# Performance work log

Hardware: AMD Instinct MI355X
Metric: run time of the kernel (lower is better)

## Reference

```python
import jax, jax.numpy as jnp
import numpy as np
from jax import lax

R = 1
EPS = 1e-4
K = 2 * R + 1


def _dir_kernels(r):
    k = 2 * r + 1
    ones = np.ones((k, k), np.float32)
    L = ones.copy(); L[:, r + 1:] = 0
    Rk = ones.copy(); Rk[:, :r] = 0
    U = ones.copy(); U[r + 1:, :] = 0
    D = ones.copy(); D[:r, :] = 0
    # NW/NE/SW/SE clone U/D BEFORE normalization (as in the torch code)
    NW = U.copy(); NW[:, r + 1:] = 0
    NE = U.copy(); NE[:, :r] = 0
    SW = D.copy(); SW[:, r + 1:] = 0
    SE = D.copy(); SE[:, :r] = 0
    half = (r + 1) * k          # normalizer for half windows
    quad = (r + 1) ** 2         # normalizer for quadrant windows
    L, Rk, U, D = L / half, Rk / half, U / half, D / half
    NW, NE, SW, SE = NW / quad, NE / quad, SW / quad, SE / quad
    return jnp.asarray(np.stack([L, Rk, U, D, NW, NE, SW, SE])[:, None])  # [8,1,k,k]


_DN = ('NCHW', 'OIHW', 'NCHW')


def _boxfilter(x, r):
    # replication pad + depthwise ones/(k*k) box filter; x: [N,3,H,W]
    k = 2 * r + 1
    xp = jnp.pad(x, ((0, 0), (0, 0), (r, r), (r, r)), mode='edge')
    w = jnp.full((3, 1, k, k), 1.0 / (k * k), dtype=x.dtype)
    return lax.conv_general_dilated(xp, w, (1, 1), 'VALID',
                                    dimension_numbers=_DN, feature_group_count=3)


def setup_inputs() -> dict:
    key = jax.random.key(0)
    k1, k2, k3 = jax.random.split(key, 3)
    lr_x = jax.random.uniform(k1, (1, 3, 2048, 2048), jnp.float32) * 255.0
    lr_y = jax.random.uniform(k2, (1, 3, 2048, 2048), jnp.float32) * 255.0
    hr_x = jax.random.uniform(k3, (1, 3, 4096, 4096), jnp.float32) * 255.0
    return {"lr_x": lr_x, "lr_y": lr_y, "hr_x": hr_x}


def reference(lr_x, lr_y, hr_x):
    # guided-filter coefficients on the low-res pair
    mean_x = _boxfilter(lr_x, R)
    mean_y = _boxfilter(lr_y, R)
    cov_xy = _boxfilter(lr_x * lr_y, R) - mean_x * mean_y
    var_x = _boxfilter(lr_x * lr_x, R) - mean_x * mean_x
    A = cov_xy / (var_x + EPS)            # [1,3,H,W]
    b = mean_y - A * mean_x               # [1,3,H,W]

    # treat channels as batch: [3,1,H,W]; 8 directional kernels at once
    Wd = _dir_kernels(R)                  # [8,1,k,k]
    A_ = A[0][:, None]
    b_ = b[0][:, None]
    im = lr_x[0][:, None]                 # [3,1,H,W]
    pad = [(R, R), (R, R)]
    convA = lax.conv_general_dilated(A_, Wd, (1, 1), pad, dimension_numbers=_DN)
    convb = lax.conv_general_dilated(b_, Wd, (1, 1), pad, dimension_numbers=_DN)
    d = convA * im + convb - im           # [3,8,H,W] directional residuals

    idx = jnp.argmin(jnp.abs(d), axis=1, keepdims=True)   # [3,1,H,W]
    dm = jnp.take_along_axis(d, idx, axis=1)              # best residual
    res = (dm + im).transpose(1, 0, 2, 3)                 # [1,3,H,W]
    # .int() truncation then clamp to [0,255], back to float
    return jnp.clip(jnp.trunc(res), 0.0, 255.0)
```

## Files before the change

### kernel.cpp

```cpp
#include <hip/hip_runtime.h>
#include <math.h>


#define TX 64
#define TY 16
#define SW (TX + 4)
#define SH (TY + 4)
#define AW (TX + 2)
#define AH (TY + 2)
#define NT 256

__device__ __forceinline__ double fast_rcp(double v) {
#if __has_builtin(__builtin_amdgcn_rcp)
    double r = __builtin_amdgcn_rcp(v);
#else
    double r = 1.0 / v;
#endif
    double e = fma(-v, r, 1.0);
    r = fma(r, e, r);
    e = fma(-v, r, 1.0);
    r = fma(r, e, r);
    return r;
}

__global__ __launch_bounds__(NT) void fgf_fused_kernel(
    const float* __restrict__ x, const float* __restrict__ y,
    float* __restrict__ out, int H, int W)
{
    __shared__ float  sxs[SH][SW];
    __shared__ float  sys[SH][SW];
    __shared__ double sA[AH][AW];
    __shared__ double sB[AH][AW];

    const int c   = blockIdx.z;
    const int ox0 = blockIdx.x * TX;
    const int oy0 = blockIdx.y * TY;
    const size_t plane = (size_t)H * (size_t)W;
    const float* xc = x + (size_t)c * plane;
    const float* yc = y + (size_t)c * plane;

    const int tid = threadIdx.y * 64 + threadIdx.x;

    for (int i = tid; i < SH * SW; i += NT) {
        int ly = i / SW, lx = i - ly * SW;
        int gy = oy0 - 2 + ly;
        int gx = ox0 - 2 + lx;
        gy = gy < 0 ? 0 : (gy >= H ? H - 1 : gy);
        gx = gx < 0 ? 0 : (gx >= W ? W - 1 : gx);
        size_t gidx = (size_t)gy * W + gx;
        sxs[ly][lx] = xc[gidx];
        sys[ly][lx] = yc[gidx];
    }
    __syncthreads();

    const double EPS81 = 81.0 * 1.0e-4;
    const double INV9  = 1.0 / 9.0;
    for (int i = tid; i < AH * AW; i += NT) {
        int ly = i / AW, lx = i - ly * AW;
        int ay = oy0 - 1 + ly;
        int ax = ox0 - 1 + lx;
        double Av = 0.0, Bv = 0.0;
        if (ay >= 0 && ay < H && ax >= 0 && ax < W) {
            double sx4 = 0.0, sy4 = 0.0, sxy = 0.0, sxx = 0.0;
#pragma unroll
            for (int dy = 0; dy < 3; dy++) {
#pragma unroll
                for (int dx = 0; dx < 3; dx++) {
                    double xv = (double)sxs[ly + dy][lx + dx];
                    double yv = (double)sys[ly + dy][lx + dx];
                    sx4 += xv;
                    sy4 += yv;
                    sxy = fma(xv, yv, sxy);
                    sxx = fma(xv, xv, sxx);
                }
            }
            double num = fma(-sx4, sy4, 9.0 * sxy);
            double den = fma(-sx4, sx4, fma(9.0, sxx, EPS81));
            Av = num * fast_rcp(den);
            Bv = fma(-Av, sx4, sy4) * INV9;
        }
        sA[ly][lx] = Av;
        sB[ly][lx] = Bv;
    }
    __syncthreads();

    const double I6 = 1.0 / 6.0;
    const int tx = threadIdx.x;
    const int g  = threadIdx.y;
    const int r0 = g * 4;
    const int xg = ox0 + tx;
    const bool xok = (xg < W);

    double tA[3], mA[3], pA[3], tB[3], mB[3], pB[3];
#pragma unroll
    for (int cc = 0; cc < 3; cc++) {
        double a0 = sA[r0 + 0][tx + cc];
        double a1 = sA[r0 + 1][tx + cc];
        double a2 = sA[r0 + 2][tx + cc];
        tA[cc] = a0 + a1; mA[cc] = a1 + a2; pA[cc] = a2;
        double b0 = sB[r0 + 0][tx + cc];
        double b1 = sB[r0 + 1][tx + cc];
        double b2 = sB[r0 + 2][tx + cc];
        tB[cc] = b0 + b1; mB[cc] = b1 + b2; pB[cc] = b2;
    }

#pragma unroll
    for (int step = 0; step < 4; step++) {
        const int r  = r0 + step;
        const int yg = oy0 + r;
        if (xok && yg < H) {
            double fA0 = tA[0] + pA[0], fA1 = tA[1] + pA[1], fA2 = tA[2] + pA[2];
            double fB0 = tB[0] + pB[0], fB1 = tB[1] + pB[1], fB2 = tB[2] + pB[2];

            double t01A = tA[0] + tA[1], t12A = tA[1] + tA[2];
            double m01A = mA[0] + mA[1], m12A = mA[1] + mA[2];
            double t01B = tB[0] + tB[1], t12B = tB[1] + tB[2];
            double m01B = mB[0] + mB[1], m12B = mB[1] + mB[2];

            double cA[8], cB[8];
            cA[0] = (fA0 + fA1) * I6;      cB[0] = (fB0 + fB1) * I6;
            cA[1] = (fA1 + fA2) * I6;      cB[1] = (fB1 + fB2) * I6;
            cA[2] = (t01A + tA[2]) * I6;   cB[2] = (t01B + tB[2]) * I6;
            cA[3] = (m01A + mA[2]) * I6;   cB[3] = (m01B + mB[2]) * I6;
            cA[4] = t01A * 0.25;           cB[4] = t01B * 0.25;
            cA[5] = t12A * 0.25;           cB[5] = t12B * 0.25;
            cA[6] = m01A * 0.25;           cB[6] = m01B * 0.25;
            cA[7] = m12A * 0.25;           cB[7] = m12B * 0.25;

            double im = (double)sxs[r + 2][tx + 2];

            double best_ad = 1.0e300, best_d = 0.0;
#pragma unroll
            for (int k = 0; k < 8; k++) {
                double d  = fma(cA[k], im, cB[k]) - im;
                double ad = fabs(d);
                if (ad < best_ad) { best_ad = ad; best_d = d; }
            }

            double res = trunc(best_d + im);
            res = fmin(fmax(res, 0.0), 255.0);
            out[(size_t)c * plane + (size_t)yg * W + xg] = (float)res;
        }

        if (step < 3) {
#pragma unroll
            for (int cc = 0; cc < 3; cc++) {
                double nA = sA[r0 + step + 3][tx + cc];
                double nB = sB[r0 + step + 3][tx + cc];
                tA[cc] = mA[cc]; mA[cc] = pA[cc] + nA; pA[cc] = nA;
                tB[cc] = mB[cc]; mB[cc] = pB[cc] + nB; pB[cc] = nB;
            }
        }
    }
}

extern "C" void kernel_launch(void* const* d_in, const int* in_sizes, int n_in,
                              void* d_out, int out_size, void* d_ws, size_t ws_size,
                              hipStream_t stream) {
    const float* lr_x = (const float*)d_in[0];
    const float* lr_y = (const float*)d_in[1];
    float* out = (float*)d_out;

    const int plane = in_sizes[0] / 3;
    const int H = (int)(0.5 + sqrt((double)plane));
    const int W = plane / H;

    dim3 block(64, 4, 1);
    dim3 grid((W + TX - 1) / TX, (H + TY - 1) / TY, 3);
    fgf_fused_kernel<<<grid, block, 0, stream>>>(lr_x, lr_y, out, H, W);
}
```

Baseline: 361.5 us.

## Use separable column sums for box statistics and reorganize directional sums

```diff
diff --git a/kernel.cpp b/kernel.cpp
--- a/kernel.cpp
+++ b/kernel.cpp
@@ -9,6 +9,11 @@
 #define AW (TX + 2)
 #define AH (TY + 2)
 #define NT 256
+
+#define NA (AH * AW)
+#define NV (AH * SW)
+#define NS (SH * SW)
+#define ITER_A ((NA + NT - 1) / NT)
 
 __device__ __forceinline__ double fast_rcp(double v) {
 #if __has_builtin(__builtin_amdgcn_rcp)
@@ -29,8 +34,7 @@
 {
     __shared__ float  sxs[SH][SW];
     __shared__ float  sys[SH][SW];
-    __shared__ double sA[AH][AW];
-    __shared__ double sB[AH][AW];
+    __shared__ double sV[4][AH][SW];
 
     const int c   = blockIdx.z;
     const int ox0 = blockIdx.x * TX;
@@ -41,7 +45,7 @@
 
     const int tid = threadIdx.y * 64 + threadIdx.x;
 
-    for (int i = tid; i < SH * SW; i += NT) {
+    for (int i = tid; i < NS; i += NT) {
         int ly = i / SW, lx = i - ly * SW;
         int gy = oy0 - 2 + ly;
         int gx = ox0 - 2 + lx;
@@ -53,36 +57,60 @@
     }
     __syncthreads();
 
+    for (int i = tid; i < NV; i += NT) {
+        int ly = i / SW, lx = i - ly * SW;
+        double x0 = (double)sxs[ly + 0][lx];
+        double x1 = (double)sxs[ly + 1][lx];
+        double x2 = (double)sxs[ly + 2][lx];
+        double y0 = (double)sys[ly + 0][lx];
+        double y1 = (double)sys[ly + 1][lx];
+        double y2 = (double)sys[ly + 2][lx];
+        sV[0][ly][lx] = (x0 + x1) + x2;
+        sV[1][ly][lx] = (y0 + y1) + y2;
+        sV[2][ly][lx] = fma(x2, y2, fma(x1, y1, x0 * y0));
+        sV[3][ly][lx] = fma(x2, x2, fma(x1, x1, x0 * x0));
+    }
+    __syncthreads();
+
     const double EPS81 = 81.0 * 1.0e-4;
     const double INV9  = 1.0 / 9.0;
-    for (int i = tid; i < AH * AW; i += NT) {
-        int ly = i / AW, lx = i - ly * AW;
-        int ay = oy0 - 1 + ly;
-        int ax = ox0 - 1 + lx;
+    double Abuf[ITER_A], Bbuf[ITER_A];
+#pragma unroll
+    for (int it = 0; it < ITER_A; it++) {
+        int i = tid + it * NT;
         double Av = 0.0, Bv = 0.0;
-        if (ay >= 0 && ay < H && ax >= 0 && ax < W) {
-            double sx4 = 0.0, sy4 = 0.0, sxy = 0.0, sxx = 0.0;
-#pragma unroll
-            for (int dy = 0; dy < 3; dy++) {
-#pragma unroll
-                for (int dx = 0; dx < 3; dx++) {
-                    double xv = (double)sxs[ly + dy][lx + dx];
-                    double yv = (double)sys[ly + dy][lx + dx];
-                    sx4 += xv;
-                    sy4 += yv;
-                    sxy = fma(xv, yv, sxy);
-                    sxx = fma(xv, xv, sxx);
-                }
+        if (i < NA) {
+            int ly = i / AW, lx = i - ly * AW;
+            int ay = oy0 - 1 + ly;
+            int ax = ox0 - 1 + lx;
+            if (ay >= 0 && ay < H && ax >= 0 && ax < W) {
+                double Sx  = (sV[0][ly][lx] + sV[0][ly][lx + 1]) + sV[0][ly][lx + 2];
+                double Sy  = (sV[1][ly][lx] + sV[1][ly][lx + 1]) + sV[1][ly][lx + 2];
+                double Sxy = (sV[2][ly][lx] + sV[2][ly][lx + 1]) + sV[2][ly][lx + 2];
+                double Sxx = (sV[3][ly][lx] + sV[3][ly][lx + 1]) + sV[3][ly][lx + 2];
+                double num = fma(9.0, Sxy, -(Sx * Sy));
+                double den = fma(-Sx, Sx, fma(9.0, Sxx, EPS81));
+                Av = num * fast_rcp(den);
+                Bv = fma(-Av, Sx, Sy) * INV9;
             }
-            double num = fma(-sx4, sy4, 9.0 * sxy);
-            double den = fma(-sx4, sx4, fma(9.0, sxx, EPS81));
-            Av = num * fast_rcp(den);
-            Bv = fma(-Av, sx4, sy4) * INV9;
-        }
-        sA[ly][lx] = Av;
-        sB[ly][lx] = Bv;
-    }
-    __syncthreads();
+        }
+        Abuf[it] = Av;
+        Bbuf[it] = Bv;
+    }
+    __syncthreads();
+#pragma unroll
+    for (int it = 0; it < ITER_A; it++) {
+        int i = tid + it * NT;
+        if (i < NA) {
+            int ly = i / AW, lx = i - ly * AW;
+            sV[0][ly][lx] = Abuf[it];
+            sV[1][ly][lx] = Bbuf[it];
+        }
+    }
+    __syncthreads();
+
+    double (*sA)[SW] = sV[0];
+    double (*sB)[SW] = sV[1];
 
     const double I6 = 1.0 / 6.0;
     const int tx = threadIdx.x;
@@ -91,17 +119,28 @@
     const int xg = ox0 + tx;
     const bool xok = (xg < W);
 
-    double tA[3], mA[3], pA[3], tB[3], mB[3], pB[3];
-#pragma unroll
-    for (int cc = 0; cc < 3; cc++) {
-        double a0 = sA[r0 + 0][tx + cc];
-        double a1 = sA[r0 + 1][tx + cc];
-        double a2 = sA[r0 + 2][tx + cc];
-        tA[cc] = a0 + a1; mA[cc] = a1 + a2; pA[cc] = a2;
-        double b0 = sB[r0 + 0][tx + cc];
-        double b1 = sB[r0 + 1][tx + cc];
-        double b2 = sB[r0 + 2][tx + cc];
-        tB[cc] = b0 + b1; mB[cc] = b1 + b2; pB[cc] = b2;
+    double tLA, tRA, tFA, mLA, mRA, mFA, pLA, pRA, pFA;
+    double tLB, tRB, tFB, mLB, mRB, mFB, pLB, pRB, pFB;
+    {
+        double a0 = sA[r0 + 0][tx], a1 = sA[r0 + 0][tx + 1], a2 = sA[r0 + 0][tx + 2];
+        double L0 = a0 + a1, R0 = a1 + a2, F0 = L0 + a2;
+        a0 = sA[r0 + 1][tx]; a1 = sA[r0 + 1][tx + 1]; a2 = sA[r0 + 1][tx + 2];
+        double L1 = a0 + a1, R1 = a1 + a2, F1 = L1 + a2;
+        a0 = sA[r0 + 2][tx]; a1 = sA[r0 + 2][tx + 1]; a2 = sA[r0 + 2][tx + 2];
+        double L2 = a0 + a1, R2 = a1 + a2, F2 = L2 + a2;
+        tLA = L0 + L1; tRA = R0 + R1; tFA = F0 + F1;
+        mLA = L1 + L2; mRA = R1 + R2; mFA = F1 + F2;
+        pLA = L2; pRA = R2; pFA = F2;
+
+        double b0 = sB[r0 + 0][tx], b1 = sB[r0 + 0][tx + 1], b2 = sB[r0 + 0][tx + 2];
+        double M0 = b0 + b1, S0 = b1 + b2, G0 = M0 + b2;
+        b0 = sB[r0 + 1][tx]; b1 = sB[r0 + 1][tx + 1]; b2 = sB[r0 + 1][tx + 2];
+        double M1 = b0 + b1, S1 = b1 + b2, G1 = M1 + b2;
+        b0 = sB[r0 + 2][tx]; b1 = sB[r0 + 2][tx + 1]; b2 = sB[r0 + 2][tx + 2];
+        double M2 = b0 + b1, S2 = b1 + b2, G2 = M2 + b2;
+        tLB = M0 + M1; tRB = S0 + S1; tFB = G0 + G1;
+        mLB = M1 + M2; mRB = S1 + S2; mFB = G1 + G2;
+        pLB = M2; pRB = S2; pFB = G2;
     }
 
 #pragma unroll
@@ -109,47 +148,38 @@
         const int r  = r0 + step;
         const int yg = oy0 + r;
         if (xok && yg < H) {
-            double fA0 = tA[0] + pA[0], fA1 = tA[1] + pA[1], fA2 = tA[2] + pA[2];
-            double fB0 = tB[0] + pB[0], fB1 = tB[1] + pB[1], fB2 = tB[2] + pB[2];
-
-            double t01A = tA[0] + tA[1], t12A = tA[1] + tA[2];
-            double m01A = mA[0] + mA[1], m12A = mA[1] + mA[2];
-            double t01B = tB[0] + tB[1], t12B = tB[1] + tB[2];
-            double m01B = mB[0] + mB[1], m12B = mB[1] + mB[2];
-
-            double cA[8], cB[8];
-            cA[0] = (fA0 + fA1) * I6;      cB[0] = (fB0 + fB1) * I6;
-            cA[1] = (fA1 + fA2) * I6;      cB[1] = (fB1 + fB2) * I6;
-            cA[2] = (t01A + tA[2]) * I6;   cB[2] = (t01B + tB[2]) * I6;
-            cA[3] = (m01A + mA[2]) * I6;   cB[3] = (m01B + mB[2]) * I6;
-            cA[4] = t01A * 0.25;           cB[4] = t01B * 0.25;
-            cA[5] = t12A * 0.25;           cB[5] = t12B * 0.25;
-            cA[6] = m01A * 0.25;           cB[6] = m01B * 0.25;
-            cA[7] = m12A * 0.25;           cB[7] = m12B * 0.25;
-
-            double im = (double)sxs[r + 2][tx + 2];
-
-            double best_ad = 1.0e300, best_d = 0.0;
+            double im  = (double)sxs[r + 2][tx + 2];
+            double mim = -im;
+
+            double sa[8] = { tLA + pLA, tRA + pRA, tFA, mFA, tLA, tRA, mLA, mRA };
+            double sb[8] = { tLB + pLB, tRB + pRB, tFB, mFB, tLB, tRB, mLB, mRB };
+
+            double best = 0.0;
 #pragma unroll
             for (int k = 0; k < 8; k++) {
-                double d  = fma(cA[k], im, cB[k]) - im;
-                double ad = fabs(d);
-                if (ad < best_ad) { best_ad = ad; best_d = d; }
+                double w = (k < 4) ? I6 : 0.25;
+                double d = fma(w, fma(sa[k], im, sb[k]), mim);
+                if (k == 0) best = d;
+                else        best = (fabs(d) < fabs(best)) ? d : best;
             }
 
-            double res = trunc(best_d + im);
+            double res = trunc(best + im);
             res = fmin(fmax(res, 0.0), 255.0);
             out[(size_t)c * plane + (size_t)yg * W + xg] = (float)res;
         }
 
         if (step < 3) {
-#pragma unroll
-            for (int cc = 0; cc < 3; cc++) {
-                double nA = sA[r0 + step + 3][tx + cc];
-                double nB = sB[r0 + step + 3][tx + cc];
-                tA[cc] = mA[cc]; mA[cc] = pA[cc] + nA; pA[cc] = nA;
-                tB[cc] = mB[cc]; mB[cc] = pB[cc] + nB; pB[cc] = nB;
-            }
+            double n0 = sA[r + 3][tx], n1 = sA[r + 3][tx + 1], n2 = sA[r + 3][tx + 2];
+            double nL = n0 + n1, nR = n1 + n2, nF = nL + n2;
+            tLA = mLA; tRA = mRA; tFA = mFA;
+            mLA = pLA + nL; mRA = pRA + nR; mFA = pFA + nF;
+            pLA = nL; pRA = nR; pFA = nF;
+
+            n0 = sB[r + 3][tx]; n1 = sB[r + 3][tx + 1]; n2 = sB[r + 3][tx + 2];
+            nL = n0 + n1; nR = n1 + n2; nF = nL + n2;
+            tLB = mLB; tRB = mRB; tFB = mFB;
+            mLB = pLB + nL; mRB = pRB + nR; mFB = pFB + nF;
+            pLB = nL; pRB = nR; pFB = nF;
         }
     }
 }
```

After: 386.9 us. 1.07x slower.

## Replace shared-memory tile with register-resident rolling row band per thread

Applied to the files above, without the earlier changes.

```diff
diff --git a/kernel.cpp b/kernel.cpp
--- a/kernel.cpp
+++ b/kernel.cpp
@@ -2,12 +2,8 @@
 #include <math.h>
 
 
-#define TX 64
+#define BX 512
 #define TY 16
-#define SW (TX + 4)
-#define SH (TY + 4)
-#define AW (TX + 2)
-#define AH (TY + 2)
 #define NT 256
 
 __device__ __forceinline__ double fast_rcp(double v) {
@@ -23,135 +19,183 @@
     return r;
 }
 
-__global__ __launch_bounds__(NT) void fgf_fused_kernel(
+__device__ __forceinline__ int iclamp(int v, int lo, int hi) {
+    return v < lo ? lo : (v > hi ? hi : v);
+}
+
+template <int P, bool EMIT, bool PREF>
+__device__ __forceinline__ void fgf_step(
+    int S, int y0, int c0, int H, int W,
+    const float* __restrict__ xc, const float* __restrict__ yc,
+    float* __restrict__ oc,
+    const int (&coli)[6], const bool (&av)[4],
+    float (&xr)[3][6], float (&yr)[3][6],
+    float (&xn)[6], float (&yn)[6],
+    double (&CA)[3][2][3], double (&CB)[3][2][3])
+{
+    const double EPS81 = 81.0 * 1.0e-4;
+    const double INV9  = 1.0 / 9.0;
+    const double I6    = 1.0 / 6.0;
+    constexpr int PO = (P + 1) % 3;
+    constexpr int PM = (P + 2) % 3;
+
+#pragma unroll
+    for (int k = 0; k < 6; k++) { xr[P][k] = xn[k]; yr[P][k] = yn[k]; }
+
+    if (PREF) {
+        int rn = y0 + S + 1; if (rn > H - 1) rn = H - 1;
+        const float* __restrict__ pxn = xc + (size_t)rn * W;
+        const float* __restrict__ pyn = yc + (size_t)rn * W;
+#pragma unroll
+        for (int k = 0; k < 6; k++) { xn[k] = pxn[coli[k]]; yn[k] = pyn[coli[k]]; }
+    }
+
+    const int ar = y0 + S - 1;
+
+    double Sx[6], Sy[6], Sxy[6], Sxx[6];
+#pragma unroll
+    for (int k = 0; k < 6; k++) {
+        double x0v = (double)xr[PO][k];
+        double x1v = (double)xr[PM][k];
+        double x2v = (double)xr[P][k];
+        double y0v = (double)yr[PO][k];
+        double y1v = (double)yr[PM][k];
+        double y2v = (double)yr[P][k];
+        Sx[k]  = (x0v + x1v) + x2v;
+        Sy[k]  = (y0v + y1v) + y2v;
+        Sxy[k] = fma(x2v, y2v, fma(x1v, y1v, x0v * y0v));
+        Sxx[k] = fma(x2v, x2v, fma(x1v, x1v, x0v * x0v));
+    }
+
+    const bool rvalid = (ar >= 0) && (ar < H);
+    double Aj[4], Bj[4];
+#pragma unroll
+    for (int j = 0; j < 4; j++) {
+        double sx3  = (Sx[j]  + Sx[j + 1])  + Sx[j + 2];
+        double sy3  = (Sy[j]  + Sy[j + 1])  + Sy[j + 2];
+        double sxy3 = (Sxy[j] + Sxy[j + 1]) + Sxy[j + 2];
+        double sxx3 = (Sxx[j] + Sxx[j + 1]) + Sxx[j + 2];
+        double num = fma(9.0, sxy3, -(sx3 * sy3));
+        double den = fma(-sx3, sx3, fma(9.0, sxx3, EPS81));
+        double Av = num * fast_rcp(den);
+        double Bv = fma(-Av, sx3, sy3) * INV9;
+        bool ok = rvalid && av[j];
+        Aj[j] = ok ? Av : 0.0;
+        Bj[j] = ok ? Bv : 0.0;
+    }
+
+#pragma unroll
+    for (int i = 0; i < 2; i++) {
+        double l = Aj[i] + Aj[i + 1], r = Aj[i + 1] + Aj[i + 2];
+        CA[P][i][0] = l; CA[P][i][1] = r; CA[P][i][2] = l + Aj[i + 2];
+        l = Bj[i] + Bj[i + 1]; r = Bj[i + 1] + Bj[i + 2];
+        CB[P][i][0] = l; CB[P][i][1] = r; CB[P][i][2] = l + Bj[i + 2];
+    }
+
+    if (EMIT) {
+        const int oy = ar - 1;
+        if (oy < H) {
+            float o0 = 0.0f, o1 = 0.0f;
+#pragma unroll
+            for (int i = 0; i < 2; i++) {
+                double im  = (double)xr[PO][i + 2];
+                double mim = -im;
+                double nwA = CA[PO][i][0] + CA[PM][i][0];
+                double neA = CA[PO][i][1] + CA[PM][i][1];
+                double sa[8] = {
+                    nwA + CA[P][i][0],
+                    neA + CA[P][i][1],
+                    CA[PO][i][2] + CA[PM][i][2],
+                    CA[PM][i][2] + CA[P][i][2],
+                    nwA,
+                    neA,
+                    CA[PM][i][0] + CA[P][i][0],
+                    CA[PM][i][1] + CA[P][i][1]
+                };
+                double nwB = CB[PO][i][0] + CB[PM][i][0];
+                double neB = CB[PO][i][1] + CB[PM][i][1];
+                double sb[8] = {
+                    nwB + CB[P][i][0],
+                    neB + CB[P][i][1],
+                    CB[PO][i][2] + CB[PM][i][2],
+                    CB[PM][i][2] + CB[P][i][2],
+                    nwB,
+                    neB,
+                    CB[PM][i][0] + CB[P][i][0],
+                    CB[PM][i][1] + CB[P][i][1]
+                };
+                double best = 0.0;
+#pragma unroll
+                for (int q = 0; q < 8; q++) {
+                    double wq = (q < 4) ? I6 : 0.25;
+                    double dq = fma(wq, fma(sa[q], im, sb[q]), mim);
+                    if (q == 0) best = dq;
+                    else best = (fabs(dq) < fabs(best)) ? dq : best;
+                }
+                double res = trunc(best + im);
+                res = fmin(fmax(res, 0.0), 255.0);
+                if (i == 0) o0 = (float)res; else o1 = (float)res;
+            }
+            size_t ob = (size_t)oy * W + c0;
+            if (c0 + 1 < W) {
+                float2 o2; o2.x = o0; o2.y = o1;
+                *reinterpret_cast<float2*>(&oc[ob]) = o2;
+            } else if (c0 < W) {
+                oc[ob] = o0;
+            }
+        }
+    }
+}
+
+__global__ __launch_bounds__(NT, 2) void fgf_band_kernel(
     const float* __restrict__ x, const float* __restrict__ y,
     float* __restrict__ out, int H, int W)
 {
-    __shared__ float  sxs[SH][SW];
-    __shared__ float  sys[SH][SW];
-    __shared__ double sA[AH][AW];
-    __shared__ double sB[AH][AW];
-
     const int c   = blockIdx.z;
-    const int ox0 = blockIdx.x * TX;
-    const int oy0 = blockIdx.y * TY;
+    const int bx0 = blockIdx.x * BX;
+    const int y0  = blockIdx.y * TY;
     const size_t plane = (size_t)H * (size_t)W;
     const float* xc = x + (size_t)c * plane;
     const float* yc = y + (size_t)c * plane;
-
-    const int tid = threadIdx.y * 64 + threadIdx.x;
-
-    for (int i = tid; i < SH * SW; i += NT) {
-        int ly = i / SW, lx = i - ly * SW;
-        int gy = oy0 - 2 + ly;
-        int gx = ox0 - 2 + lx;
-        gy = gy < 0 ? 0 : (gy >= H ? H - 1 : gy);
-        gx = gx < 0 ? 0 : (gx >= W ? W - 1 : gx);
-        size_t gidx = (size_t)gy * W + gx;
-        sxs[ly][lx] = xc[gidx];
-        sys[ly][lx] = yc[gidx];
-    }
-    __syncthreads();
-
-    const double EPS81 = 81.0 * 1.0e-4;
-    const double INV9  = 1.0 / 9.0;
-    for (int i = tid; i < AH * AW; i += NT) {
-        int ly = i / AW, lx = i - ly * AW;
-        int ay = oy0 - 1 + ly;
-        int ax = ox0 - 1 + lx;
-        double Av = 0.0, Bv = 0.0;
-        if (ay >= 0 && ay < H && ax >= 0 && ax < W) {
-            double sx4 = 0.0, sy4 = 0.0, sxy = 0.0, sxx = 0.0;
-#pragma unroll
-            for (int dy = 0; dy < 3; dy++) {
-#pragma unroll
-                for (int dx = 0; dx < 3; dx++) {
-                    double xv = (double)sxs[ly + dy][lx + dx];
-                    double yv = (double)sys[ly + dy][lx + dx];
-                    sx4 += xv;
-                    sy4 += yv;
-                    sxy = fma(xv, yv, sxy);
-                    sxx = fma(xv, xv, sxx);
-                }
-            }
-            double num = fma(-sx4, sy4, 9.0 * sxy);
-            double den = fma(-sx4, sx4, fma(9.0, sxx, EPS81));
-            Av = num * fast_rcp(den);
-            Bv = fma(-Av, sx4, sy4) * INV9;
+    float* oc = out + (size_t)c * plane;
+
+    const int t  = threadIdx.y * 64 + threadIdx.x;
+    const int c0 = bx0 + 2 * t;
+
+    int coli[6];
+    bool av[4];
+#pragma unroll
+    for (int k = 0; k < 6; k++) coli[k] = iclamp(c0 - 2 + k, 0, W - 1);
+#pragma unroll
+    for (int j = 0; j < 4; j++) { int ax = c0 - 1 + j; av[j] = (ax >= 0) && (ax < W); }
+
+    float  xr[3][6], yr[3][6], xn[6], yn[6];
+    double CA[3][2][3], CB[3][2][3];
+
+    {
+        int r1 = iclamp(y0 - 2, 0, H - 1);
+        int r2 = iclamp(y0 - 1, 0, H - 1);
+        const float* px1 = xc + (size_t)r1 * W;  const float* py1 = yc + (size_t)r1 * W;
+        const float* px2 = xc + (size_t)r2 * W;  const float* py2 = yc + (size_t)r2 * W;
+        const float* px3 = xc + (size_t)y0 * W;  const float* py3 = yc + (size_t)y0 * W;
+#pragma unroll
+        for (int k = 0; k < 6; k++) {
+            xr[1][k] = px1[coli[k]]; yr[1][k] = py1[coli[k]];
+            xr[2][k] = px2[coli[k]]; yr[2][k] = py2[coli[k]];
+            xn[k]    = px3[coli[k]]; yn[k]    = py3[coli[k]];
         }
-        sA[ly][lx] = Av;
-        sB[ly][lx] = Bv;
-    }
-    __syncthreads();
-
-    const double I6 = 1.0 / 6.0;
-    const int tx = threadIdx.x;
-    const int g  = threadIdx.y;
-    const int r0 = g * 4;
-    const int xg = ox0 + tx;
-    const bool xok = (xg < W);
-
-    double tA[3], mA[3], pA[3], tB[3], mB[3], pB[3];
-#pragma unroll
-    for (int cc = 0; cc < 3; cc++) {
-        double a0 = sA[r0 + 0][tx + cc];
-        double a1 = sA[r0 + 1][tx + cc];
-        double a2 = sA[r0 + 2][tx + cc];
-        tA[cc] = a0 + a1; mA[cc] = a1 + a2; pA[cc] = a2;
-        double b0 = sB[r0 + 0][tx + cc];
-        double b1 = sB[r0 + 1][tx + cc];
-        double b2 = sB[r0 + 2][tx + cc];
-        tB[cc] = b0 + b1; mB[cc] = b1 + b2; pB[cc] = b2;
-    }
-
-#pragma unroll
-    for (int step = 0; step < 4; step++) {
-        const int r  = r0 + step;
-        const int yg = oy0 + r;
-        if (xok && yg < H) {
-            double fA0 = tA[0] + pA[0], fA1 = tA[1] + pA[1], fA2 = tA[2] + pA[2];
-            double fB0 = tB[0] + pB[0], fB1 = tB[1] + pB[1], fB2 = tB[2] + pB[2];
-
-            double t01A = tA[0] + tA[1], t12A = tA[1] + tA[2];
-            double m01A = mA[0] + mA[1], m12A = mA[1] + mA[2];
-            double t01B = tB[0] + tB[1], t12B = tB[1] + tB[2];
-            double m01B = mB[0] + mB[1], m12B = mB[1] + mB[2];
-
-            double cA[8], cB[8];
-            cA[0] = (fA0 + fA1) * I6;      cB[0] = (fB0 + fB1) * I6;
-            cA[1] = (fA1 + fA2) * I6;      cB[1] = (fB1 + fB2) * I6;
-            cA[2] = (t01A + tA[2]) * I6;   cB[2] = (t01B + tB[2]) * I6;
-            cA[3] = (m01A + mA[2]) * I6;   cB[3] = (m01B + mB[2]) * I6;
-            cA[4] = t01A * 0.25;           cB[4] = t01B * 0.25;
-            cA[5] = t12A * 0.25;           cB[5] = t12B * 0.25;
-            cA[6] = m01A * 0.25;           cB[6] = m01B * 0.25;
-            cA[7] = m12A * 0.25;           cB[7] = m12B * 0.25;
-
-            double im = (double)sxs[r + 2][tx + 2];
-
-            double best_ad = 1.0e300, best_d = 0.0;
-#pragma unroll
-            for (int k = 0; k < 8; k++) {
-                double d  = fma(cA[k], im, cB[k]) - im;
-                double ad = fabs(d);
-                if (ad < best_ad) { best_ad = ad; best_d = d; }
-            }
-
-            double res = trunc(best_d + im);
-            res = fmin(fmax(res, 0.0), 255.0);
-            out[(size_t)c * plane + (size_t)yg * W + xg] = (float)res;
-        }
-
-        if (step < 3) {
-#pragma unroll
-            for (int cc = 0; cc < 3; cc++) {
-                double nA = sA[r0 + step + 3][tx + cc];
-                double nB = sB[r0 + step + 3][tx + cc];
-                tA[cc] = mA[cc]; mA[cc] = pA[cc] + nA; pA[cc] = nA;
-                tB[cc] = mB[cc]; mB[cc] = pB[cc] + nB; pB[cc] = nB;
-            }
-        }
-    }
+    }
+
+    fgf_step<0, false, true>(0, y0, c0, H, W, xc, yc, oc, coli, av, xr, yr, xn, yn, CA, CB);
+    fgf_step<1, false, true>(1, y0, c0, H, W, xc, yc, oc, coli, av, xr, yr, xn, yn, CA, CB);
+#pragma unroll 1
+    for (int sb = 0; sb < 5; sb++) {
+        const int S2 = 2 + 3 * sb;
+        fgf_step<2, true, true>(S2,     y0, c0, H, W, xc, yc, oc, coli, av, xr, yr, xn, yn, CA, CB);
+        fgf_step<0, true, true>(S2 + 1, y0, c0, H, W, xc, yc, oc, coli, av, xr, yr, xn, yn, CA, CB);
+        fgf_step<1, true, true>(S2 + 2, y0, c0, H, W, xc, yc, oc, coli, av, xr, yr, xn, yn, CA, CB);
+    }
+    fgf_step<2, true, false>(17, y0, c0, H, W, xc, yc, oc, coli, av, xr, yr, xn, yn, CA, CB);
 }
 
 extern "C" void kernel_launch(void* const* d_in, const int* in_sizes, int n_in,
@@ -166,6 +210,6 @@
     const int W = plane / H;
 
     dim3 block(64, 4, 1);
-    dim3 grid((W + TX - 1) / TX, (H + TY - 1) / TY, 3);
-    fgf_fused_kernel<<<grid, block, 0, stream>>>(lr_x, lr_y, out, H, W);
-}
+    dim3 grid((W + BX - 1) / BX, (H + TY - 1) / TY, 3);
+    fgf_band_kernel<<<grid, block, 0, stream>>>(lr_x, lr_y, out, H, W);
+}
```

New measurement: 348.4 us. 1.04x faster.
